# Performance work log

Measured on AMD Instinct MI355X. Metric: run time of the kernel, lower is better.

The kernel has to match this reference:

```python
import jax, jax.numpy as jnp
import numpy as np

N, K, D = 32768, 8192, 512

def setup_inputs() -> dict:
    key = jax.random.key(0)
    kx, kw = jax.random.split(key)
    x = jax.random.normal(kx, (N, D), dtype=jnp.float32)
    # nn.Embedding weight init: uniform(-1/K, 1/K)
    codebook = jax.random.uniform(kw, (K, D), dtype=jnp.float32, minval=-1.0 / K, maxval=1.0 / K)
    return {"x": x, "codebook": codebook}

def reference(x, codebook):
    distances = (
        jnp.sum(x * x, axis=1, keepdims=True)
        + jnp.sum(codebook * codebook, axis=1)
        - 2.0 * jnp.einsum("nd,kd->nk", x, codebook)
    )
    encoding_indices = jnp.argmin(distances, axis=1)            # [N]
    encodings = jax.nn.one_hot(encoding_indices, K, dtype=x.dtype)  # [N, K]
    quantized = jnp.einsum("nk,kd->nd", encodings, codebook)    # [N, D]
    return quantized, encodings, encoding_indices
```

## Files before the change

### kernel.cpp

```cpp
#include <hip/hip_runtime.h>
#include <hip/hip_fp8.h>
#include <stdint.h>

#define D     512
#define BM    128
#define BN    128
#define BKC   128
#define CAND  96
#define MARGIN 7e-4f
#define MARGINS (8192.0f * MARGIN)
#define KDIM  8192

typedef __attribute__((ext_vector_type(4))) float f32x4;

__device__ __forceinline__ unsigned char f2fp8(float f) {
  __hip_fp8_e4m3 q(f);
  return (unsigned char)q.__x;
}

__device__ __forceinline__ unsigned fkey(float f) {
  unsigned u = __float_as_uint(f);
  return (u >> 31) ? ~u : (u | 0x80000000u);
}
__device__ __forceinline__ float unfkey(unsigned k) {
  unsigned u = (k >> 31) ? (k & 0x7FFFFFFFu) : ~k;
  return __uint_as_float(u);
}

__global__ __launch_bounds__(256) void vq_prep(const float* __restrict__ cb,
                                               unsigned char* __restrict__ w8,
                                               float* __restrict__ b32, int K) {
  int wid  = blockIdx.x * 4 + (threadIdx.x >> 6);
  int lane = threadIdx.x & 63;
  if (wid >= K) return;
  const float* row = cb + (size_t)wid * D + lane * 8;
  float4 a = *(const float4*)row;
  float4 b = *(const float4*)(row + 4);
  float v[8] = {a.x, a.y, a.z, a.w, b.x, b.y, b.z, b.w};
  double s = 0.0;
  unsigned long long p = 0ull;
#pragma unroll
  for (int j = 0; j < 8; ++j) {
    float sq = v[j] * v[j]; s += (double)sq;
    p |= (unsigned long long)f2fp8(v[j] * 8192.0f) << (8 * j);
  }
  *(unsigned long long*)(w8 + (size_t)wid * D + lane * 8) = p;
#pragma unroll
  for (int m = 1; m < 64; m <<= 1) s += __shfl_xor(s, m);
  if (lane == 0) b32[wid] = (float)s;
}

__device__ __forceinline__ void stage2(const unsigned char* __restrict__ w8,
                                       unsigned char (*wb)[BN * BKC], int kt2, int c2,
                                       int w, int lane) {
#pragma unroll
  for (int i = 0; i < 2; ++i) {
    const int sb  = (w * 2 + i) * 64;
    const int s   = sb + lane;
    const int row = s >> 3;
    const int j   = s & 7;
    const int k16 = j ^ (row & 7);
    const unsigned char* src = w8 + (size_t)(kt2 * BN + row) * D + c2 * BKC + k16 * 16;
    unsigned char* dst = &wb[c2][sb * 16];
    __builtin_amdgcn_global_load_lds(
        (const __attribute__((address_space(1))) unsigned int*)src,
        (__attribute__((address_space(3))) unsigned int*)dst, 16, 0, 0);
  }
}

__global__ __launch_bounds__(512, 2) void vq_main(
    const float* __restrict__ x, const float* __restrict__ cb,
    const unsigned char* __restrict__ w8, const float* __restrict__ b32g,
    float* __restrict__ out_q, float* __restrict__ out_enc, float* __restrict__ out_idx,
    int N, int K) {
  __shared__ unsigned char wb[4][BN * BKC];
  __shared__ unsigned rowmin[BM];
  __shared__ unsigned rowcnt[BM];
  __shared__ unsigned candb[BM][CAND];

  const int t    = threadIdx.x;
  const int lane = t & 63;
  const int w    = t >> 6;
  const int wr   = w >> 1;
  const int wc   = w & 1;
  const int l15  = lane & 15;
  const int l16  = lane >> 4;
  const int m_base = blockIdx.x * BM;
  const int nkt  = K / BN;
  float* const enc_blk = out_enc + (size_t)m_base * K;

  if (t < BM) { rowmin[t] = 0xFFFFFFFFu; rowcnt[t] = 0u; }

  stage2(w8, wb, 0, 0, w, lane);
  stage2(w8, wb, 0, 1, w, lane);

  long afr[2][16];
#pragma unroll
  for (int mi = 0; mi < 2; ++mi) {
    const float* xr = x + (size_t)(m_base + 32 * wr + 16 * mi + l15) * D;
#pragma unroll
    for (int f = 0; f < 16; ++f) {
      const float* p = xr + f * 32 + l16 * 8;
      float4 a = *(const float4*)p;
      float4 b = *(const float4*)(p + 4);
      float v[8] = {a.x, a.y, a.z, a.w, b.x, b.y, b.z, b.w};
      unsigned long long pk = 0ull;
#pragma unroll
      for (int j = 0; j < 8; ++j) pk |= (unsigned long long)f2fp8(v[j]) << (8 * j);
      afr[mi][f] = (long)pk;
    }
  }
  __syncthreads();

  for (int kt = 0; kt < nkt; ++kt) {
    float b32v[4];
#pragma unroll
    for (int ni = 0; ni < 4; ++ni)
      b32v[ni] = 8192.0f * b32g[kt * BN + 64 * wc + 16 * ni + l15];

    f32x4 acc[2][4];
#pragma unroll
    for (int mi = 0; mi < 2; ++mi)
#pragma unroll
      for (int ni = 0; ni < 4; ++ni) acc[mi][ni] = (f32x4){0.f, 0.f, 0.f, 0.f};

#pragma unroll
    for (int c = 0; c < 4; ++c) {
      const int kt2 = kt + ((c + 2) >> 2);
      if (kt2 < nkt) stage2(w8, wb, kt2, (c + 2) & 3, w, lane);
      {
        const f32x4 z4 = {0.f, 0.f, 0.f, 0.f};
        f32x4* ez = (f32x4*)(enc_blk + (size_t)kt * (BM * KDIM / 64));
        __builtin_nontemporal_store(z4, ez + (c * 2 + 0) * 512 + t);
        __builtin_nontemporal_store(z4, ez + (c * 2 + 1) * 512 + t);
      }

      const unsigned char* wp = &wb[c][0];
      __builtin_amdgcn_s_setprio(1);
#pragma unroll
      for (int ks = 0; ks < 4; ++ks) {
        long bfr[4];
#pragma unroll
        for (int ni = 0; ni < 4; ++ni) {
          const int row  = 64 * wc + 16 * ni + l15;
          const int slot = (ks * 2 + (l16 >> 1)) ^ (row & 7);
          bfr[ni] = *(const long*)(wp + row * BKC + slot * 16 + (l16 & 1) * 8);
        }
#pragma unroll
        for (int mi = 0; mi < 2; ++mi)
#pragma unroll
          for (int ni = 0; ni < 4; ++ni)
            acc[mi][ni] = __builtin_amdgcn_mfma_f32_16x16x32_fp8_fp8(
                afr[mi][c * 4 + ks], bfr[ni], acc[mi][ni], 0, 0, 0);
      }
      __builtin_amdgcn_s_setprio(0);
      if (kt2 < nkt) asm volatile("s_waitcnt vmcnt(4)" ::: "memory");
      else           asm volatile("s_waitcnt vmcnt(0)" ::: "memory");
      __builtin_amdgcn_sched_barrier(0);
      __builtin_amdgcn_s_barrier();
    }

    float tv[2][4][4];
#pragma unroll
    for (int mi = 0; mi < 2; ++mi)
#pragma unroll
      for (int ni = 0; ni < 4; ++ni)
#pragma unroll
        for (int r = 0; r < 4; ++r)
          tv[mi][ni][r] = fmaf(-2.0f, acc[mi][ni][r], b32v[ni]);

    if (kt == 0) {
#pragma unroll
      for (int mi = 0; mi < 2; ++mi)
#pragma unroll
        for (int r = 0; r < 4; ++r) {
          float m = fminf(fminf(tv[mi][0][r], tv[mi][1][r]),
                          fminf(tv[mi][2][r], tv[mi][3][r]));
          atomicMin(&rowmin[32 * wr + 16 * mi + 4 * l16 + r], fkey(m));
        }
      __syncthreads();
    }

#pragma unroll
    for (int mi = 0; mi < 2; ++mi) {
      const int rbase = 32 * wr + 16 * mi + 4 * l16;
      const uint4 ru = *(const uint4*)&rowmin[rbase];
      const unsigned rua[4] = {ru.x, ru.y, ru.z, ru.w};
#pragma unroll
      for (int r = 0; r < 4; ++r) {
        const float rm  = unfkey(rua[r]);
        const float thr = rm + MARGINS;
        const float mn  = fminf(fminf(tv[mi][0][r], tv[mi][1][r]),
                                fminf(tv[mi][2][r], tv[mi][3][r]));
        if (mn < rm) atomicMin(&rowmin[rbase + r], fkey(mn));
#pragma unroll
        for (int ni = 0; ni < 4; ++ni) {
          if (tv[mi][ni][r] <= thr) {
            unsigned p = atomicAdd(&rowcnt[rbase + r], 1u);
            if (p < CAND) candb[rbase + r][p] = (unsigned)(kt * BN + 64 * wc + 16 * ni + l15);
          }
        }
      }
    }
  }
  __syncthreads();

  for (int r = w; r < BM; r += 8) {
    const int n = m_base + r;
    const float* xr = x + (size_t)n * D + lane * 8;
    float4 xa = *(const float4*)xr;
    float4 xb = *(const float4*)(xr + 4);
    float xv[8] = {xa.x, xa.y, xa.z, xa.w, xb.x, xb.y, xb.z, xb.w};
    double s = 0.0;
#pragma unroll
    for (int j = 0; j < 8; ++j) { float sq = xv[j] * xv[j]; s += (double)sq; }
#pragma unroll
    for (int m = 1; m < 64; m <<= 1) s += __shfl_xor(s, m);
    const float Arow = (float)s;

    const unsigned c = rowcnt[r];
    const bool uselist = (c >= 1u && c <= (unsigned)CAND);
    const int nc = uselist ? (int)c : K;
    unsigned long long best = 0xFFFFFFFFFFFFFFFFull;
    for (int i = 0; i < nc; ++i) {
      const int k = uselist ? (int)candb[r][i] : i;
      const float* wp = cb + (size_t)k * D + lane * 8;
      float4 wa = *(const float4*)wp;
      float4 wbv = *(const float4*)(wp + 4);
      float wv[8] = {wa.x, wa.y, wa.z, wa.w, wbv.x, wbv.y, wbv.z, wbv.w};
      double d = 0.0;
#pragma unroll
      for (int j = 0; j < 8; ++j) d += (double)xv[j] * (double)wv[j];
#pragma unroll
      for (int m = 1; m < 64; m <<= 1) d += __shfl_xor(d, m);
      const float C32 = (float)d;
      const float T1  = Arow + b32g[k];
      const float sc  = T1 - 2.0f * C32;
      unsigned long long pk = ((unsigned long long)__float_as_uint(sc) << 32) | (unsigned)k;
      best = best < pk ? best : pk;
    }
    const int kstar = (int)(best & 0xFFFFFFFFu);

    if (lane == 0) {
      out_idx[n] = (float)kstar;
      out_enc[(size_t)n * K + kstar] = 1.0f;
    }
    const float* qs = cb + (size_t)kstar * D + lane * 8;
    float4 q0 = *(const float4*)qs;
    float4 q1 = *(const float4*)(qs + 4);
    f32x4* qd = (f32x4*)(out_q + (size_t)n * D + lane * 8);
    f32x4 q0v = {q0.x, q0.y, q0.z, q0.w};
    f32x4 q1v = {q1.x, q1.y, q1.z, q1.w};
    __builtin_nontemporal_store(q0v, qd);
    __builtin_nontemporal_store(q1v, qd + 1);
  }
}

extern "C" void kernel_launch(void* const* d_in, const int* in_sizes, int n_in,
                              void* d_out, int out_size, void* d_ws, size_t ws_size,
                              hipStream_t stream) {
  const float* x  = (const float*)d_in[0];
  const float* cb = (const float*)d_in[1];
  const int N = in_sizes[0] / D;
  const int K = in_sizes[1] / D;

  unsigned char* w8 = (unsigned char*)d_ws;
  float* b32 = (float*)((char*)d_ws + (size_t)K * D);

  float* out     = (float*)d_out;
  float* out_q   = out;
  float* out_enc = out + (size_t)N * D;
  float* out_idx = out + (size_t)N * D + (size_t)N * K;

  vq_prep<<<(K + 3) / 4, 256, 0, stream>>>(cb, w8, b32, K);
  vq_main<<<N / BM, 512, 0, stream>>>(x, cb, w8, b32, out_q, out_enc, out_idx, N, K);
}
```

Measured before the change: 502.1 us.

## Store approximate scores with candidates and rescore four candidates per wave

```diff
diff --git a/kernel.cpp b/kernel.cpp
--- a/kernel.cpp
+++ b/kernel.cpp
@@ -6,12 +6,13 @@
 #define BM    128
 #define BN    128
 #define BKC   128
-#define CAND  96
+#define CAND  64
 #define MARGIN 7e-4f
 #define MARGINS (8192.0f * MARGIN)
 #define KDIM  8192
 
 typedef __attribute__((ext_vector_type(4))) float f32x4;
+typedef unsigned long long u64;
 
 __device__ __forceinline__ unsigned char f2fp8(float f) {
   __hip_fp8_e4m3 q(f);
@@ -38,13 +39,13 @@
   float4 b = *(const float4*)(row + 4);
   float v[8] = {a.x, a.y, a.z, a.w, b.x, b.y, b.z, b.w};
   double s = 0.0;
-  unsigned long long p = 0ull;
+  u64 p = 0ull;
 #pragma unroll
   for (int j = 0; j < 8; ++j) {
     float sq = v[j] * v[j]; s += (double)sq;
-    p |= (unsigned long long)f2fp8(v[j] * 8192.0f) << (8 * j);
-  }
-  *(unsigned long long*)(w8 + (size_t)wid * D + lane * 8) = p;
+    p |= (u64)f2fp8(v[j] * 8192.0f) << (8 * j);
+  }
+  *(u64*)(w8 + (size_t)wid * D + lane * 8) = p;
 #pragma unroll
   for (int m = 1; m < 64; m <<= 1) s += __shfl_xor(s, m);
   if (lane == 0) b32[wid] = (float)s;
@@ -76,7 +77,7 @@
   __shared__ unsigned char wb[4][BN * BKC];
   __shared__ unsigned rowmin[BM];
   __shared__ unsigned rowcnt[BM];
-  __shared__ unsigned candb[BM][CAND];
+  __shared__ u64 candb[BM][CAND];
 
   const int t    = threadIdx.x;
   const int lane = t & 63;
@@ -104,9 +105,9 @@
       float4 a = *(const float4*)p;
       float4 b = *(const float4*)(p + 4);
       float v[8] = {a.x, a.y, a.z, a.w, b.x, b.y, b.z, b.w};
-      unsigned long long pk = 0ull;
-#pragma unroll
-      for (int j = 0; j < 8; ++j) pk |= (unsigned long long)f2fp8(v[j]) << (8 * j);
+      u64 pk = 0ull;
+#pragma unroll
+      for (int j = 0; j < 8; ++j) pk |= (u64)f2fp8(v[j]) << (8 * j);
       afr[mi][f] = (long)pk;
     }
   }
@@ -154,7 +155,7 @@
                 afr[mi][c * 4 + ks], bfr[ni], acc[mi][ni], 0, 0, 0);
       }
       __builtin_amdgcn_s_setprio(0);
-      if (kt2 < nkt) asm volatile("s_waitcnt vmcnt(4)" ::: "memory");
+      if (kt2 < nkt) asm volatile("s_waitcnt vmcnt(6)" ::: "memory");
       else           asm volatile("s_waitcnt vmcnt(0)" ::: "memory");
       __builtin_amdgcn_sched_barrier(0);
       __builtin_amdgcn_s_barrier();
@@ -197,7 +198,9 @@
         for (int ni = 0; ni < 4; ++ni) {
           if (tv[mi][ni][r] <= thr) {
             unsigned p = atomicAdd(&rowcnt[rbase + r], 1u);
-            if (p < CAND) candb[rbase + r][p] = (unsigned)(kt * BN + 64 * wc + 16 * ni + l15);
+            if (p < CAND)
+              candb[rbase + r][p] = ((u64)fkey(tv[mi][ni][r]) << 32)
+                                  | (unsigned)(kt * BN + 64 * wc + 16 * ni + l15);
           }
         }
       }
@@ -207,37 +210,58 @@
 
   for (int r = w; r < BM; r += 8) {
     const int n = m_base + r;
-    const float* xr = x + (size_t)n * D + lane * 8;
-    float4 xa = *(const float4*)xr;
-    float4 xb = *(const float4*)(xr + 4);
-    float xv[8] = {xa.x, xa.y, xa.z, xa.w, xb.x, xb.y, xb.z, xb.w};
+    const float* xr = x + (size_t)n * D + l15 * 32;
+    float xv[32];
+#pragma unroll
+    for (int j4 = 0; j4 < 8; ++j4) {
+      float4 v = *(const float4*)(xr + j4 * 4);
+      xv[j4 * 4 + 0] = v.x; xv[j4 * 4 + 1] = v.y;
+      xv[j4 * 4 + 2] = v.z; xv[j4 * 4 + 3] = v.w;
+    }
     double s = 0.0;
 #pragma unroll
-    for (int j = 0; j < 8; ++j) { float sq = xv[j] * xv[j]; s += (double)sq; }
-#pragma unroll
-    for (int m = 1; m < 64; m <<= 1) s += __shfl_xor(s, m);
+    for (int j = 0; j < 32; ++j) { float sq = xv[j] * xv[j]; s += (double)sq; }
+#pragma unroll
+    for (int m = 1; m < 16; m <<= 1) s += __shfl_xor(s, m);
     const float Arow = (float)s;
 
-    const unsigned c = rowcnt[r];
-    const bool uselist = (c >= 1u && c <= (unsigned)CAND);
-    const int nc = uselist ? (int)c : K;
-    unsigned long long best = 0xFFFFFFFFFFFFFFFFull;
-    for (int i = 0; i < nc; ++i) {
-      const int k = uselist ? (int)candb[r][i] : i;
-      const float* wp = cb + (size_t)k * D + lane * 8;
-      float4 wa = *(const float4*)wp;
-      float4 wbv = *(const float4*)(wp + 4);
-      float wv[8] = {wa.x, wa.y, wa.z, wa.w, wbv.x, wbv.y, wbv.z, wbv.w};
-      double d = 0.0;
-#pragma unroll
-      for (int j = 0; j < 8; ++j) d += (double)xv[j] * (double)wv[j];
-#pragma unroll
-      for (int m = 1; m < 64; m <<= 1) d += __shfl_xor(d, m);
-      const float C32 = (float)d;
-      const float T1  = Arow + b32g[k];
-      const float sc  = T1 - 2.0f * C32;
-      unsigned long long pk = ((unsigned long long)__float_as_uint(sc) << 32) | (unsigned)k;
-      best = best < pk ? best : pk;
+    const unsigned cgot = rowcnt[r];
+    const bool uselist = (cgot >= 1u && cgot <= (unsigned)CAND);
+    const int nc = uselist ? (int)cgot : K;
+    const float thrF = unfkey(rowmin[r]) + MARGINS;
+    u64 best = 0xFFFFFFFFFFFFFFFFull;
+
+    for (int i = 0; i < nc; i += 4) {
+      const int ci = i + l16;
+      if (ci < nc) {
+        int k; bool ok = true;
+        if (uselist) {
+          const u64 e = candb[r][ci];
+          k = (int)(e & 0xFFFFFFFFu);
+          ok = (unfkey((unsigned)(e >> 32)) <= thrF);
+        } else k = ci;
+        if (ok) {
+          const float* wp = cb + (size_t)k * D + l15 * 32;
+          double d = 0.0;
+#pragma unroll
+          for (int j4 = 0; j4 < 8; ++j4) {
+            float4 v = *(const float4*)(wp + j4 * 4);
+            d += (double)xv[j4 * 4 + 0] * v.x; d += (double)xv[j4 * 4 + 1] * v.y;
+            d += (double)xv[j4 * 4 + 2] * v.z; d += (double)xv[j4 * 4 + 3] * v.w;
+          }
+#pragma unroll
+          for (int m = 1; m < 16; m <<= 1) d += __shfl_xor(d, m);
+          const float C32 = (float)d;
+          const float T1  = Arow + b32g[k];
+          const float sc  = T1 - 2.0f * C32;
+          const u64 pk = ((u64)__float_as_uint(sc) << 32) | (unsigned)k;
+          best = best < pk ? best : pk;
+        }
+      }
+    }
+    {
+      u64 o = __shfl_xor(best, 16); best = best < o ? best : o;
+      o     = __shfl_xor(best, 32); best = best < o ? best : o;
     }
     const int kstar = (int)(best & 0xFFFFFFFFu);
 
```

New measurement: 489.5 us. 1.03x faster.
